# Performance work log

Measured on AMD Instinct MI355X. Metric: run time of the kernel, lower is better.

Reference implementation:

```python
import jax, jax.numpy as jnp
import numpy as np

SEQ, D_IN, D_KQ, D_V = 4096, 1024, 1024, 1024

def setup_inputs() -> dict:
    key = jax.random.key(0)
    k1, k2, k3, k4 = jax.random.split(key, 4)
    return {
        "x": jax.random.normal(k1, (SEQ, D_IN), dtype=jnp.float32),
        "W_query": jax.random.uniform(k2, (D_IN, D_KQ), dtype=jnp.float32),
        "W_key": jax.random.uniform(k3, (D_IN, D_KQ), dtype=jnp.float32),
        "W_value": jax.random.uniform(k4, (D_IN, D_V), dtype=jnp.float32),
    }

def reference(x, W_query, W_key, W_value):
    d_out_kq = W_query.shape[1]
    Q = x @ W_query          # [S, d_kq]
    K = x @ W_key            # [S, d_kq]
    V = x @ W_value          # [S, d_v]
    attn = Q @ K.T           # [S, S]
    S = attn.shape[0]
    causal_mask = jnp.triu(jnp.ones((S, S), dtype=bool), k=1)
    masked = jnp.where(causal_mask, -jnp.inf, attn)
    attn_weights = jax.nn.softmax(masked / jnp.sqrt(jnp.float32(d_out_kq)), axis=1)
    return attn_weights @ V  # [S, d_v]
```

## Files before the change

kernel.cpp:

```cpp
#include <hip/hip_runtime.h>
#include <math.h>

#define SQ 4096
#define DD 1024
#define TRI 528

typedef _Float16 f16;
typedef f16 f16x8 __attribute__((ext_vector_type(8)));
typedef f16 f16x4 __attribute__((ext_vector_type(4)));
typedef float f32x4 __attribute__((ext_vector_type(4)));

__device__ __forceinline__ float waveMax(float v) {
#pragma unroll
    for (int o = 32; o > 0; o >>= 1) v = fmaxf(v, __shfl_down(v, o, 64));
    return v;
}
__device__ __forceinline__ float waveSum(float v) {
#pragma unroll
    for (int o = 32; o > 0; o >>= 1) v += __shfl_down(v, o, 64);
    return v;
}

__device__ __forceinline__ void gl_lds16(const f16* g, f16* l) {
    __builtin_amdgcn_global_load_lds(
        (const __attribute__((address_space(1))) void*)g,
        (__attribute__((address_space(3))) void*)l, 16, 0, 0);
}

template<int NRW>
__device__ __forceinline__ void stage(const f16* src, int ldk, f16* lds, int w, int lane) {
    const int r0 = w * NRW + (lane >> 2);
    const f16* g = src + (size_t)r0 * ldk + ((lane & 3) << 3);
    f16* l = lds + w * NRW * 32;
    gl_lds16(g, l);
    if (NRW == 32) gl_lds16(g + (size_t)ldk * 16, l + 16 * 32);
}

template<int MODE>
__global__ __launch_bounds__(256)
void gemm_k(const f16* __restrict__ Ah, const f16* __restrict__ Al,
            const f16* __restrict__ Bh, const f16* __restrict__ Bl,
            float* __restrict__ Cf,
            f16* __restrict__ Qh, f16* __restrict__ Ql,
            f16* __restrict__ Kh, f16* __restrict__ Kl,
            f16* __restrict__ Vt, float scale)
{
    constexpr int TM = (MODE == 2) ? 64 : 128;
    constexpr int NI = (MODE == 2) ? 2 : 4;
    constexpr int H  = (MODE == 2) ? 2 : 1;
    constexpr int AH = TM * 32;
    constexpr int BH = 128 * 32;
    constexpr bool HAS_AL = (MODE != 2);
    constexpr bool HAS_BL = (MODE == 1);
    constexpr int SMSZ = H * AH + H * BH + (HAS_AL ? H * AH : 0) + (HAS_BL ? H * BH : 0);

    int bm, bn, tri = 0, half = 0;
    if (MODE == 1) {
        const int lin = blockIdx.x;
        half = lin & 1;
        tri = lin >> 1;
        bm = (int)((sqrtf(8.f * (float)tri + 1.f) - 1.f) * 0.5f);
        while ((bm + 1) * (bm + 2) / 2 <= tri) ++bm;
        while (bm * (bm + 1) / 2 > tri) --bm;
        bn = tri - bm * (bm + 1) / 2;
    } else if (MODE == 2) {
        bm = 63 - (int)blockIdx.x;
        bn = blockIdx.y;
    } else {
        bn = blockIdx.x; bm = blockIdx.y;
    }

    const int m0 = bm * TM;
    const int n0 = bn << 7;
    const int lda = (MODE == 2) ? 128 : DD;
    const int ldb = (MODE == 2) ? SQ : DD;
    const int kst = (MODE == 1) ? (half << 9) : 0;
    const int kend = (MODE == 1) ? (kst + 512)
                   : (MODE == 2) ? (((bm >> 1) + 1) << 7) : DD;
    const bool aLo = (MODE == 1) || (MODE == 0 && bn < 16);

    __shared__ f16 sm[SMSZ];
    f16* smA  = sm;
    f16* smB  = sm + H * AH;
    f16* smAl = smB + H * BH;
    f16* smBl = smAl + (HAS_AL ? H * AH : 0);

    const int tid = threadIdx.x;
    const int w = tid >> 6, lane = tid & 63;
    const int wr = (MODE == 2) ? 0 : ((w >> 1) << 6);
    const int wc = (MODE == 2) ? (w << 5) : ((w & 1) << 6);
    const int fcol = lane & 15, quad = lane >> 4;

    f32x4 acc[4][NI];
#pragma unroll
    for (int i = 0; i < 4; ++i)
#pragma unroll
        for (int j = 0; j < NI; ++j) acc[i][j] = (f32x4){0.f, 0.f, 0.f, 0.f};

    const int bmT = (MODE == 2) ? (bm >> 1) : 0;
    const size_t triRow = (MODE == 2) ? (size_t)(bmT * (bmT + 1) / 2) : 0;
    const f16* Bb  = Bh + (size_t)n0 * ldb;
    const f16* Abl = (HAS_AL && aLo) ? Al + (size_t)m0 * DD : nullptr;
    const f16* Bbl = HAS_BL ? Bl + (size_t)n0 * ldb : nullptr;

    for (int k0 = kst; k0 < kend; k0 += 32 * H) {
        __syncthreads();
#pragma unroll
        for (int h = 0; h < H; ++h) {
            const int kk = k0 + 32 * h;
            const f16* as;
            if (MODE == 2) {
                as = Ah + ((triRow + (size_t)(kk >> 7)) << 14)
                        + ((size_t)(m0 & 127) << 7) + (kk & 127);
            } else {
                as = Ah + (size_t)m0 * DD + kk;
            }
            stage<TM / 4>(as, lda, smA + h * AH, w, lane);
            stage<32>(Bb + kk, ldb, smB + h * BH, w, lane);
            if (HAS_AL && aLo) stage<TM / 4>(Abl + kk, DD, smAl + h * AH, w, lane);
            if (HAS_BL)        stage<32>(Bbl + kk, ldb, smBl + h * BH, w, lane);
        }
        __syncthreads();

#pragma unroll
        for (int h = 0; h < H; ++h) {
            f16x8 bh[NI], bl[NI];
#pragma unroll
            for (int in = 0; in < NI; ++in) {
                const int off = ((wc + (in << 4) + fcol) << 5) + (quad << 3);
                bh[in] = *(const f16x8*)&smB[h * BH + off];
                if (HAS_BL) bl[in] = *(const f16x8*)&smBl[h * BH + off];
            }
#pragma unroll
            for (int im = 0; im < 4; ++im) {
                const int off = ((wr + (im << 4) + fcol) << 5) + (quad << 3);
                f16x8 ah = *(const f16x8*)&smA[h * AH + off];
                f16x8 al;
                if (HAS_AL && aLo) al = *(const f16x8*)&smAl[h * AH + off];
#pragma unroll
                for (int in = 0; in < NI; ++in) {
                    if (HAS_BL)
                        acc[im][in] = __builtin_amdgcn_mfma_f32_16x16x32_f16(ah, bl[in], acc[im][in], 0, 0, 0);
                    if (HAS_AL && aLo)
                        acc[im][in] = __builtin_amdgcn_mfma_f32_16x16x32_f16(al, bh[in], acc[im][in], 0, 0, 0);
                    acc[im][in] = __builtin_amdgcn_mfma_f32_16x16x32_f16(ah, bh[in], acc[im][in], 0, 0, 0);
                }
            }
        }
    }

#pragma unroll
    for (int im = 0; im < 4; ++im) {
#pragma unroll
        for (int in = 0; in < NI; ++in) {
            if (MODE == 0) {
                const int region = bn >> 3;
                const int colL = ((bn & 7) << 7) + wc + (in << 4) + fcol;
                if (region == 2) {
                    const int tc = m0 + wr + (im << 4) + (quad << 2);
                    f16x4 o;
#pragma unroll
                    for (int r = 0; r < 4; ++r) o[r] = (f16)acc[im][in][r];
                    *(f16x4*)&Vt[(size_t)colL * SQ + tc] = o;
                } else {
                    f16* Hh = region ? Kh : Qh;
                    f16* Hl = region ? Kl : Ql;
#pragma unroll
                    for (int r = 0; r < 4; ++r) {
                        const int row = m0 + wr + (im << 4) + (quad << 2) + r;
                        const float v = acc[im][in][r];
                        const f16 h = (f16)v;
                        Hh[(size_t)row * DD + colL] = h;
                        Hl[(size_t)row * DD + colL] = (f16)(v - (float)h);
                    }
                }
            } else if (MODE == 1) {
                float* Cp = Cf + (((size_t)half * TRI + tri) << 14);
#pragma unroll
                for (int r = 0; r < 4; ++r) {
                    const int rl = wr + (im << 4) + (quad << 2) + r;
                    const int cl = wc + (in << 4) + fcol;
                    Cp[(rl << 7) + cl] = acc[im][in][r] * scale;
                }
            } else {
#pragma unroll
                for (int r = 0; r < 4; ++r) {
                    const int row = m0 + wr + (im << 4) + (quad << 2) + r;
                    const int col = n0 + wc + (in << 4) + fcol;
                    Cf[(size_t)row * DD + col] = acc[im][in][r];
                }
            }
        }
    }
}

__global__ __launch_bounds__(256)
void prepass(const float* __restrict__ x,
             const float* __restrict__ W0, const float* __restrict__ W1,
             const float* __restrict__ W2,
             f16* __restrict__ xh, f16* __restrict__ xl,
             f16* __restrict__ Th0)
{
    __shared__ float t[64][65];
    const int id = blockIdx.x;
    const int tid = threadIdx.x;

    if (id < 4096) {
        const int i = (id * 256 + tid) * 4;
        const float4 v = *(const float4*)(x + i);
        const f16 h0 = (f16)v.x, h1 = (f16)v.y, h2 = (f16)v.z, h3 = (f16)v.w;
        f16x4 hv = {h0, h1, h2, h3};
        f16x4 lv = {(f16)(v.x - (float)h0), (f16)(v.y - (float)h1),
                    (f16)(v.z - (float)h2), (f16)(v.w - (float)h3)};
        *(f16x4*)(xh + i) = hv;
        *(f16x4*)(xl + i) = lv;
        return;
    }

    const int tt = id - 4096;
    const int z = tt >> 8, r8 = tt & 255;
    const float* W = (z == 0) ? W0 : (z == 1) ? W1 : W2;
    f16* Th = Th0 + (size_t)z * DD * DD;
    const int n0 = (r8 & 15) << 6, k0 = (r8 >> 4) << 6;
    const int tx = tid & 63, ty = tid >> 6;
    for (int r = ty; r < 64; r += 4) t[r][tx] = W[(size_t)(k0 + r) * DD + n0 + tx];
    __syncthreads();
    for (int r = ty; r < 64; r += 4)
        Th[(size_t)(n0 + r) * DD + k0 + tx] = (f16)t[tx][r];
}

__global__ __launch_bounds__(256)
void softmax_causal(const float* __restrict__ A0, f16* __restrict__ P)
{
    const int i = blockIdx.x;
    const int n = i + 1;
    const int tid = threadIdx.x, w = tid >> 6, lane = tid & 63;
    __shared__ float redM[4], redS[4];
    __shared__ float rowbuf[SQ];

    const int bmI = i >> 7;
    const size_t base = ((size_t)(bmI * (bmI + 1) / 2) << 14) + ((size_t)(i & 127) << 7);
    const float* A1 = A0 + ((size_t)TRI << 14);

    const int nv = n >> 2;
    float m = -INFINITY;
    for (int g = tid; g < nv; g += 256) {
        const int j = g << 2;
        const size_t a = base + ((size_t)(j >> 7) << 14) + (j & 127);
        const float4 v0 = *(const float4*)(A0 + a);
        const float4 v1 = *(const float4*)(A1 + a);
        float4 v = make_float4(v0.x + v1.x, v0.y + v1.y, v0.z + v1.z, v0.w + v1.w);
        *(f32x4*)&rowbuf[j] = (f32x4){v.x, v.y, v.z, v.w};
        m = fmaxf(m, fmaxf(fmaxf(v.x, v.y), fmaxf(v.z, v.w)));
    }
    for (int j = (nv << 2) + tid; j < n; j += 256) {
        const size_t a = base + ((size_t)(j >> 7) << 14) + (j & 127);
        const float v = A0[a] + A1[a];
        rowbuf[j] = v;
        m = fmaxf(m, v);
    }
    m = waveMax(m);
    if (lane == 0) redM[w] = m;
    __syncthreads();
    const float mAll = fmaxf(fmaxf(redM[0], redM[1]), fmaxf(redM[2], redM[3]));

    float s = 0.f;
    for (int g = tid; g < nv; g += 256) {
        const int j = g << 2;
        f32x4 v = *(f32x4*)&rowbuf[j];
        v[0] = __expf(v[0] - mAll); v[1] = __expf(v[1] - mAll);
        v[2] = __expf(v[2] - mAll); v[3] = __expf(v[3] - mAll);
        *(f32x4*)&rowbuf[j] = v;
        s += v[0] + v[1] + v[2] + v[3];
    }
    for (int j = (nv << 2) + tid; j < n; j += 256) {
        const float e = __expf(rowbuf[j] - mAll);
        rowbuf[j] = e;
        s += e;
    }
    s = waveSum(s);
    if (lane == 0) redS[w] = s;
    __syncthreads();
    const float inv = 1.0f / (redS[0] + redS[1] + redS[2] + redS[3]);

    const int kmax = (bmI + 1) << 7;
    for (int g = tid; g < nv; g += 256) {
        const int j = g << 2;
        const size_t a = base + ((size_t)(j >> 7) << 14) + (j & 127);
        const f32x4 v = *(const f32x4*)&rowbuf[j];
        f16x4 o = {(f16)(v[0] * inv), (f16)(v[1] * inv),
                   (f16)(v[2] * inv), (f16)(v[3] * inv)};
        *(f16x4*)&P[a] = o;
    }
    for (int j = (nv << 2) + tid; j < kmax; j += 256) {
        const size_t a = base + ((size_t)(j >> 7) << 14) + (j & 127);
        P[a] = (j < n) ? (f16)(rowbuf[j] * inv) : (f16)0.f;
    }
}

extern "C" void kernel_launch(void* const* d_in, const int* in_sizes, int n_in,
                              void* d_out, int out_size, void* d_ws, size_t ws_size,
                              hipStream_t stream)
{
    const float* x  = (const float*)d_in[0];
    const float* Wq = (const float*)d_in[1];
    const float* Wk = (const float*)d_in[2];
    const float* Wv = (const float*)d_in[3];
    float* out = (float*)d_out;

    char* p = (char*)d_ws;
    auto take = [&](size_t bytes) { void* r = (void*)p; p += (bytes + 255) & ~(size_t)255; return r; };
    const size_t SD = (size_t)SQ * DD;
    f16* xh  = (f16*)take(SD * 2);
    f16* xl  = (f16*)take(SD * 2);
    f16* Wth = (f16*)take((size_t)3 * DD * DD * 2);
    f16* Qh  = (f16*)take(SD * 2);
    f16* Ql  = (f16*)take(SD * 2);
    f16* Kh  = (f16*)take(SD * 2);
    f16* Kl  = (f16*)take(SD * 2);
    f16* Vt  = (f16*)take(SD * 2);
    float* attn = (float*)take((size_t)2 * TRI * 16384 * 4);
    f16* P   = (f16*)take((size_t)TRI * 16384 * 2);

    const dim3 blk(256);

    prepass<<<dim3(4096 + 768), blk, 0, stream>>>(x, Wq, Wk, Wv, xh, xl, Wth);

    gemm_k<0><<<dim3(24, SQ / 128), blk, 0, stream>>>(
        xh, xl, Wth, nullptr, nullptr, Qh, Ql, Kh, Kl, Vt, 1.0f);

    gemm_k<1><<<dim3(2 * TRI), blk, 0, stream>>>(
        Qh, Ql, Kh, Kl, attn, nullptr, nullptr, nullptr, nullptr, nullptr, 0.03125f);

    softmax_causal<<<dim3(SQ), blk, 0, stream>>>(attn, P);

    gemm_k<2><<<dim3(SQ / 64, DD / 128), blk, 0, stream>>>(
        P, nullptr, Vt, nullptr, out, nullptr, nullptr, nullptr, nullptr, nullptr, 1.0f);
}
```

Before: 289.1 us.

## Use 256x128 tiles for causal QK^T GEMM to raise operand reuse

Measured after the change: 272.2 us. -5.8%, faster.

```diff
diff --git a/kernel.cpp b/kernel.cpp
--- a/kernel.cpp
+++ b/kernel.cpp
@@ -32,12 +32,13 @@
     const int r0 = w * NRW + (lane >> 2);
     const f16* g = src + (size_t)r0 * ldk + ((lane & 3) << 3);
     f16* l = lds + w * NRW * 32;
-    gl_lds16(g, l);
-    if (NRW == 32) gl_lds16(g + (size_t)ldk * 16, l + 16 * 32);
+#pragma unroll
+    for (int i = 0; i < NRW / 16; ++i)
+        gl_lds16(g + (size_t)ldk * (i << 4), l + (i << 4) * 32);
 }
 
 template<int MODE>
-__global__ __launch_bounds__(256)
+__global__ __launch_bounds__(256, 2)
 void gemm_k(const f16* __restrict__ Ah, const f16* __restrict__ Al,
             const f16* __restrict__ Bh, const f16* __restrict__ Bl,
             float* __restrict__ Cf,
@@ -45,7 +46,8 @@
             f16* __restrict__ Kh, f16* __restrict__ Kl,
             f16* __restrict__ Vt, float scale)
 {
-    constexpr int TM = (MODE == 2) ? 64 : 128;
+    constexpr int TM = (MODE == 0) ? 128 : (MODE == 1) ? 256 : 64;
+    constexpr int MI = (MODE == 1) ? 8 : 4;
     constexpr int NI = (MODE == 2) ? 2 : 4;
     constexpr int H  = (MODE == 2) ? 2 : 1;
     constexpr int AH = TM * 32;
@@ -54,15 +56,15 @@
     constexpr bool HAS_BL = (MODE == 1);
     constexpr int SMSZ = H * AH + H * BH + (HAS_AL ? H * AH : 0) + (HAS_BL ? H * BH : 0);
 
-    int bm, bn, tri = 0, half = 0;
+    int bm, bn, half = 0;
     if (MODE == 1) {
         const int lin = blockIdx.x;
         half = lin & 1;
-        tri = lin >> 1;
-        bm = (int)((sqrtf(8.f * (float)tri + 1.f) - 1.f) * 0.5f);
-        while ((bm + 1) * (bm + 2) / 2 <= tri) ++bm;
-        while (bm * (bm + 1) / 2 > tri) --bm;
-        bn = tri - bm * (bm + 1) / 2;
+        const int t = lin >> 1;
+        bm = (int)((sqrtf(4.f * (float)t + 1.f) - 1.f) * 0.5f);
+        while ((bm + 1) * (bm + 2) <= t) ++bm;
+        while (bm * bm + bm > t) --bm;
+        bn = t - bm * bm - bm;
     } else if (MODE == 2) {
         bm = 63 - (int)blockIdx.x;
         bn = blockIdx.y;
@@ -87,13 +89,14 @@
 
     const int tid = threadIdx.x;
     const int w = tid >> 6, lane = tid & 63;
-    const int wr = (MODE == 2) ? 0 : ((w >> 1) << 6);
+    const int wr = (MODE == 0) ? ((w >> 1) << 6)
+                 : (MODE == 1) ? ((w >> 1) << 7) : 0;
     const int wc = (MODE == 2) ? (w << 5) : ((w & 1) << 6);
     const int fcol = lane & 15, quad = lane >> 4;
 
-    f32x4 acc[4][NI];
-#pragma unroll
-    for (int i = 0; i < 4; ++i)
+    f32x4 acc[MI][NI];
+#pragma unroll
+    for (int i = 0; i < MI; ++i)
 #pragma unroll
         for (int j = 0; j < NI; ++j) acc[i][j] = (f32x4){0.f, 0.f, 0.f, 0.f};
 
@@ -132,7 +135,7 @@
                 if (HAS_BL) bl[in] = *(const f16x8*)&smBl[h * BH + off];
             }
 #pragma unroll
-            for (int im = 0; im < 4; ++im) {
+            for (int im = 0; im < MI; ++im) {
                 const int off = ((wr + (im << 4) + fcol) << 5) + (quad << 3);
                 f16x8 ah = *(const f16x8*)&smA[h * AH + off];
                 f16x8 al;
@@ -149,11 +152,11 @@
         }
     }
 
-#pragma unroll
-    for (int im = 0; im < 4; ++im) {
-#pragma unroll
-        for (int in = 0; in < NI; ++in) {
-            if (MODE == 0) {
+    if (MODE == 0) {
+#pragma unroll
+        for (int im = 0; im < MI; ++im) {
+#pragma unroll
+            for (int in = 0; in < NI; ++in) {
                 const int region = bn >> 3;
                 const int colL = ((bn & 7) << 7) + wc + (in << 4) + fcol;
                 if (region == 2) {
@@ -174,15 +177,31 @@
                         Hl[(size_t)row * DD + colL] = (f16)(v - (float)h);
                     }
                 }
-            } else if (MODE == 1) {
-                float* Cp = Cf + (((size_t)half * TRI + tri) << 14);
-#pragma unroll
-                for (int r = 0; r < 4; ++r) {
-                    const int rl = wr + (im << 4) + (quad << 2) + r;
+            }
+        }
+    } else if (MODE == 1) {
+        const int R = (bm << 1) + (w >> 1);
+        if (bn <= R) {
+            const int slot = ((R * (R + 1)) >> 1) + bn;
+            float* Cp = Cf + (((size_t)half * TRI + slot) << 14);
+#pragma unroll
+            for (int im = 0; im < MI; ++im) {
+#pragma unroll
+                for (int in = 0; in < NI; ++in) {
                     const int cl = wc + (in << 4) + fcol;
-                    Cp[(rl << 7) + cl] = acc[im][in][r] * scale;
+#pragma unroll
+                    for (int r = 0; r < 4; ++r) {
+                        const int rloc = (im << 4) + (quad << 2) + r;
+                        Cp[(rloc << 7) + cl] = acc[im][in][r] * scale;
+                    }
                 }
-            } else {
+            }
+        }
+    } else {
+#pragma unroll
+        for (int im = 0; im < MI; ++im) {
+#pragma unroll
+            for (int in = 0; in < NI; ++in) {
 #pragma unroll
                 for (int r = 0; r < 4; ++r) {
                     const int row = m0 + wr + (im << 4) + (quad << 2) + r;
@@ -329,7 +348,7 @@
     gemm_k<0><<<dim3(24, SQ / 128), blk, 0, stream>>>(
         xh, xl, Wth, nullptr, nullptr, Qh, Ql, Kh, Kl, Vt, 1.0f);
 
-    gemm_k<1><<<dim3(2 * TRI), blk, 0, stream>>>(
+    gemm_k<1><<<dim3(544), blk, 0, stream>>>(
         Qh, Ql, Kh, Kl, attn, nullptr, nullptr, nullptr, nullptr, nullptr, 0.03125f);
 
     softmax_causal<<<dim3(SQ), blk, 0, stream>>>(attn, P);
```
